# Kernel optimization log

Measured on AMD Instinct MI355X. Metric: run time of the kernel, lower is better.

## Reference

```python
import jax, jax.numpy as jnp
import numpy as np

EPS = 1e-08
PARTIAL_NORM = 1.5
TOPK = 8
SELF_MOD_STEPS = 2


def _layernorm(x, g, b, eps=1e-05):
    mu = jnp.mean(x, axis=-1, keepdims=True)
    var = jnp.mean((x - mu) ** 2, axis=-1, keepdims=True)
    return (x - mu) / jnp.sqrt(var + eps) * g + b


def _spectral_normalize(w, iters=10):
    # mimic torch spectral_norm: divide by top singular value (power iteration)
    u = jnp.ones((w.shape[0],), w.dtype) / np.sqrt(w.shape[0])
    def step(u, _):
        v = w.T @ u
        v = v / (jnp.linalg.norm(v) + 1e-12)
        u2 = w @ v
        u2 = u2 / (jnp.linalg.norm(u2) + 1e-12)
        return u2, None
    u, _ = jax.lax.scan(step, u, None, length=iters)
    v = w.T @ u
    v = v / (jnp.linalg.norm(v) + 1e-12)
    sigma = u @ (w @ v)
    return w / sigma


def setup_inputs() -> dict:
    B, D, H, S, C = 8192, 2048, 1024, 3, 1000
    P = 1024  # proj_dim = ((max(H, D//2)+7)//8)*8
    key = jax.random.key(0)
    ks = jax.random.split(key, 16)
    x = jax.random.normal(ks[0], (B, D), jnp.float32)
    proj_w = jax.random.normal(ks[1], (P, D), jnp.float32) / np.sqrt(D)
    proj_b = jnp.zeros((P,), jnp.float32)
    ln_p_g = jnp.ones((P,), jnp.float32)
    ln_p_b = jnp.zeros((P,), jnp.float32)
    wf_w = jax.random.normal(ks[2], (S, 2 * H, P), jnp.float32) / np.sqrt(P)
    wf_w = jax.vmap(_spectral_normalize)(wf_w)
    wf_b = jax.random.normal(ks[3], (S, 2 * H), jnp.float32) * 0.02
    ln_g = jnp.ones((S, 2 * H), jnp.float32)
    ln_b = jnp.zeros((S, 2 * H), jnp.float32)
    temperature = jnp.ones((1,), jnp.float32)
    phases = jax.random.normal(ks[4], (S, 1), jnp.float32) * 0.5
    gate_w = jax.random.normal(ks[5], (H, H), jnp.float32) / np.sqrt(H)
    gate_b = jnp.zeros((H,), jnp.float32)
    cls_w1 = jax.random.normal(ks[6], (H, H), jnp.float32) / np.sqrt(H)
    cls_b1 = jnp.zeros((H,), jnp.float32)
    cls_w2 = jax.random.normal(ks[7], (C, H), jnp.float32) / np.sqrt(H)
    cls_b2 = jnp.zeros((C,), jnp.float32).at[1].set(0.75)
    return {"x": x, "proj_w": proj_w, "proj_b": proj_b, "ln_p_g": ln_p_g,
            "ln_p_b": ln_p_b, "wf_w": wf_w, "wf_b": wf_b, "ln_g": ln_g,
            "ln_b": ln_b, "temperature": temperature, "phases": phases,
            "gate_w": gate_w, "gate_b": gate_b, "cls_w1": cls_w1,
            "cls_b1": cls_b1, "cls_w2": cls_w2, "cls_b2": cls_b2}


def reference(x, proj_w, proj_b, ln_p_g, ln_p_b, wf_w, wf_b, ln_g, ln_b,
              temperature, phases, gate_w, gate_b, cls_w1, cls_b1, cls_w2, cls_b2):
    H = wf_w.shape[1] // 2
    # input projection (dropout is identity at eval)
    h = jax.nn.gelu(_layernorm(x @ proj_w.T + proj_b, ln_p_g, ln_p_b), approximate=False)
    # all wavefunctions at once: [B, S, 2H]
    out = jnp.einsum('bp,sep->bse', h, wf_w) + wf_b[None]
    out = _layernorm(out, ln_g[None], ln_b[None])
    out = jnp.exp(-out * out)  # ArcBell
    alpha, beta = out[..., :H], out[..., H:]
    norm_sq = jnp.sum(alpha ** 2 + beta ** 2, axis=-1, keepdims=True) + EPS
    factor = jnp.sqrt(PARTIAL_NORM ** 2 / norm_sq)
    alpha = alpha * factor
    beta = beta * factor
    phase = phases[None]  # [1, S, 1]
    c, s = jnp.cos(phase), jnp.sin(phase)
    wave_r = alpha * c - beta * s  # [B, S, H]
    wave_i = alpha * s + beta * c
    # cosine-similarity interference weights
    mean_real = jnp.mean(wave_r, axis=1)  # [B, H]
    mean_norm = jnp.sqrt(jnp.sum(mean_real ** 2, axis=-1, keepdims=True)) + EPS  # [B,1]
    wave_norms = jnp.sqrt(jnp.sum(wave_r ** 2, axis=-1, keepdims=True)) + EPS  # [B,S,1]
    dot = jnp.sum(wave_r * mean_real[:, None], axis=-1, keepdims=True)  # [B,S,1]
    cos_sim = (dot / (wave_norms * mean_norm[:, None]))[..., 0]  # [B,S]
    w = jax.nn.softmax(cos_sim / temperature, axis=1)[..., None]  # [B,S,1]
    sup_r = jnp.sum(wave_r * w, axis=1)  # [B,H]
    sup_i = jnp.sum(wave_i * w, axis=1)
    # self-modulation with leaky residual
    for _ in range(SELF_MOD_STEPS):
        mag = jnp.sqrt(sup_r ** 2 + sup_i ** 2 + EPS)
        gate = jax.nn.sigmoid(mag @ gate_w.T + gate_b)
        sup_r = sup_r * gate + sup_r * 0.1
        sup_i = sup_i * gate + sup_i * 0.1
    mag_sq = sup_r ** 2 + sup_i ** 2
    # top-k mask + scatter + renormalize
    _, inds = jax.lax.top_k(mag_sq, TOPK)
    rows = jnp.arange(mag_sq.shape[0])[:, None]
    mask = jnp.zeros_like(mag_sq).at[rows, inds].set(1.0)
    masked = mag_sq * mask
    probs = masked / (jnp.sum(masked, axis=-1, keepdims=True) + EPS)
    # classifier (dropout identity at eval)
    hid = jax.nn.gelu(probs @ cls_w1.T + cls_b1, approximate=False)
    logits = hid @ cls_w2.T + cls_b2
    return logits
```

## Files before the change

kernel.cpp:

```cpp
#include <hip/hip_runtime.h>
#include <cstdint>

typedef __attribute__((ext_vector_type(8))) __bf16 bf16x8;
typedef __attribute__((ext_vector_type(4))) __bf16 bf16x4;
typedef __attribute__((ext_vector_type(4))) float f32x4;
typedef unsigned long long u64;

__device__ __forceinline__ void gld_lds16(const void* g, void* l) {
  __builtin_amdgcn_global_load_lds(
      (const __attribute__((address_space(1))) void*)g,
      (__attribute__((address_space(3))) void*)l, 16, 0, 0);
}

__device__ __forceinline__ float block_sum(float v, float* scr) {
#pragma unroll
  for (int off = 32; off > 0; off >>= 1) v += __shfl_down(v, off, 64);
  const int w = threadIdx.x >> 6;
  __syncthreads();
  if ((threadIdx.x & 63) == 0) scr[w] = v;
  __syncthreads();
  float s = 0.f;
  const int nw = blockDim.x >> 6;
  for (int i = 0; i < nw; ++i) s += scr[i];
  return s;
}

__device__ __forceinline__ float gelu_fast(float x) {
  const float ax = fabsf(x) * 0.70710678118654752f;
  const float t = 1.f / (1.f + 0.3275911f * ax);
  const float e = __expf(-ax * ax);
  float poly = 1.061405429f;
  poly = poly * t - 1.453152027f;
  poly = poly * t + 1.421413741f;
  poly = poly * t - 0.284496736f;
  poly = poly * t + 0.254829592f;
  const float erfax = 1.f - poly * t * e;
  const float er = copysignf(erfax, x);
  return 0.5f * x * (1.f + er);
}

__global__ __launch_bounds__(256) void k_cast_bf16(const float* __restrict__ in,
                                                   __bf16* __restrict__ out) {
  const long i = ((long)blockIdx.x * 256 + threadIdx.x) * 4;
  f32x4 v = *(const f32x4*)(in + i);
  bf16x4 o = {(__bf16)v[0], (__bf16)v[1], (__bf16)v[2], (__bf16)v[3]};
  *(bf16x4*)(out + i) = o;
}

__global__ __launch_bounds__(256) void k_cast_pad(const float* __restrict__ in,
                                                  __bf16* __restrict__ out,
                                                  int rows_real, int cols) {
  const long i = ((long)blockIdx.x * 256 + threadIdx.x) * 4;
  const int row = (int)(i / cols);
  const int col = (int)(i % cols);
  bf16x4 o;
  if (row < rows_real) {
    f32x4 v = *(const f32x4*)(in + (long)row * cols + col);
    o = (bf16x4){(__bf16)v[0], (__bf16)v[1], (__bf16)v[2], (__bf16)v[3]};
  } else {
    o = (bf16x4){(__bf16)0.f, (__bf16)0.f, (__bf16)0.f, (__bf16)0.f};
  }
  *(bf16x4*)(out + i) = o;
}

__global__ __launch_bounds__(256) void k_transpose1k(const float* __restrict__ in,
                                                     float* __restrict__ out) {
  __shared__ float t[32][33];
  const int tx = threadIdx.x & 31;
  const int ty = threadIdx.x >> 5;
  const int r0 = blockIdx.y * 32, c0 = blockIdx.x * 32;
#pragma unroll
  for (int k = 0; k < 4; ++k)
    t[ty + 8 * k][tx] = in[(long)(r0 + ty + 8 * k) * 1024 + c0 + tx];
  __syncthreads();
#pragma unroll
  for (int k = 0; k < 4; ++k)
    out[(long)(c0 + ty + 8 * k) * 1024 + r0 + tx] = t[tx][ty + 8 * k];
}

__global__ __launch_bounds__(512, 1) void k_gemm256_bt(
    const __bf16* __restrict__ A, const __bf16* __restrict__ B,
    const float* __restrict__ bias, __bf16* __restrict__ C,
    int M, int N, int K) {
  __shared__ __align__(16) __bf16 lds[2][2][256 * 64];
  const int tid = threadIdx.x;
  const int lane = tid & 63;
  const int wid = tid >> 6;
  const int wr = wid >> 2;
  const int wc = wid & 3;
  const int gx = gridDim.x, gy = gridDim.y;
  const int nwg = gx * gy;
  const int lin = blockIdx.y * gx + blockIdx.x;
  const int cpx = nwg >> 3;
  const int wsw = (lin & 7) * cpx + (lin >> 3);
  const int bx = wsw / gy, by = wsw % gy;
  const int m0 = by * 256, n0 = bx * 256;
  const int fr = lane & 15;
  const int fx = lane >> 4;
  const int px = lane & 7;

  const __bf16* Abase = A + (long)m0 * K;
  const __bf16* Bbase = B + (long)n0 * K;

  auto stage_q = [&](int slot, int kt, int mat, int half) {
    const __bf16* src = (mat ? Bbase : Abase) + kt * 64;
#pragma unroll
    for (int q = 0; q < 2; ++q) {
      const int idx = q * 512 + tid;
      const int r = idx >> 3;
      const int pblk = idx & 7;
      const int row = half * 128 + r;
      const int lblk = pblk ^ (r & 7);
      gld_lds16(src + (long)row * K + lblk * 8,
                (char*)&lds[slot][mat][row * 64 + pblk * 8]);
    }
  };
  auto frag = [&](int slot, int mat, int row, int ks) -> bf16x8 {
    return *(const bf16x8*)&lds[slot][mat][row * 64 + ((((ks << 2) + fx) ^ px) << 3)];
  };

  f32x4 acc[8][4] = {};
  const int nt = K >> 6;
#pragma unroll
  for (int qp = 0; qp < 4; ++qp) stage_q(0, 0, qp >> 1, qp & 1);

  const int arow = wr * 128 + fr;
  const int brow = wc * 64 + fr;

  for (int t = 0; t < nt; ++t) {
    const int sc = t & 1, sn = sc ^ 1;
    if (t + 1 < nt) {
#pragma unroll
      for (int qp = 0; qp < 4; ++qp) stage_q(sn, t + 1, qp >> 1, qp & 1);
      asm volatile("s_waitcnt vmcnt(8)" ::: "memory");
    } else {
      asm volatile("s_waitcnt vmcnt(0)" ::: "memory");
    }
    __builtin_amdgcn_sched_barrier(0);
    __builtin_amdgcn_s_barrier();
    bf16x8 b0[4], b1[4];
#pragma unroll
    for (int j = 0; j < 4; ++j) {
      b0[j] = frag(sc, 1, brow + j * 16, 0);
      b1[j] = frag(sc, 1, brow + j * 16, 1);
    }
    __builtin_amdgcn_s_setprio(1);
#pragma unroll
    for (int im = 0; im < 8; ++im) {
      bf16x8 x0 = frag(sc, 0, arow + im * 16, 0);
      bf16x8 x1 = frag(sc, 0, arow + im * 16, 1);
#pragma unroll
      for (int j = 0; j < 4; ++j) {
        acc[im][j] = __builtin_amdgcn_mfma_f32_16x16x32_bf16(x0, b0[j], acc[im][j], 0, 0, 0);
        acc[im][j] = __builtin_amdgcn_mfma_f32_16x16x32_bf16(x1, b1[j], acc[im][j], 0, 0, 0);
      }
    }
    __builtin_amdgcn_s_setprio(0);
    __builtin_amdgcn_s_barrier();
  }

  const int crow0 = m0 + wr * 128 + fx * 4;
  const int ccol0 = n0 + wc * 64 + fr;
#pragma unroll
  for (int j = 0; j < 4; ++j) {
    const int col = ccol0 + j * 16;
    const float bv = bias[col];
#pragma unroll
    for (int im = 0; im < 8; ++im)
#pragma unroll
      for (int r = 0; r < 4; ++r)
        C[(long)(crow0 + im * 16 + r) * N + col] = (__bf16)(acc[im][j][r] + bv);
  }
}

template <int EPI, int BM>
__global__ __launch_bounds__(256) void k_gemm_bt(
    const __bf16* __restrict__ A, const __bf16* __restrict__ B,
    const float* __restrict__ bias, void* __restrict__ Cout,
    int M, int N, int K, int Nreal,
    float* __restrict__ supR, float* __restrict__ supI,
    __bf16* __restrict__ magOut) {
  constexpr int MR = BM / 32;
  __shared__ __align__(16) __bf16 As[2][BM * 32];
  __shared__ __align__(16) __bf16 Bs[2][128 * 32];
  const int tid = threadIdx.x;
  const int lane = tid & 63;
  const int wid = tid >> 6;
  const int wr = wid >> 1, wc = wid & 1;

  const int gx = gridDim.x, gy = gridDim.y;
  const int nwg = gx * gy;
  int bx, by;
  if ((nwg & 7) == 0) {
    const int lin = blockIdx.y * gx + blockIdx.x;
    const int cpx = nwg >> 3;
    const int w = (lin & 7) * cpx + (lin >> 3);
    bx = w / gy;
    by = w % gy;
  } else {
    bx = blockIdx.x;
    by = blockIdx.y;
  }
  const int m0 = by * BM;
  const int n0 = bx * 128;
  const int frow = lane & 15;
  const int fk = (lane >> 4) * 8;
  f32x4 acc[MR][4] = {};

  auto stage = [&](int buf, int k0) {
    const __bf16* Ab = A + (long)m0 * K + k0;
    const __bf16* Bb = B + (long)n0 * K + k0;
#pragma unroll
    for (int q = 0; q < BM / 64; ++q) {
      const int idx = q * 256 + tid;
      const int row = idx >> 2;
      const int col = (idx & 3) * 8;
      gld_lds16(Ab + (long)row * K + col, (char*)(&As[buf][0]) + idx * 16);
    }
#pragma unroll
    for (int q = 0; q < 2; ++q) {
      const int idx = q * 256 + tid;
      const int row = idx >> 2;
      const int col = (idx & 3) * 8;
      gld_lds16(Bb + (long)row * K + col, (char*)(&Bs[buf][0]) + idx * 16);
    }
  };

  const int nt = K >> 5;
  int cur = 0;
  stage(0, 0);
  __syncthreads();
  for (int t = 0; t < nt; ++t) {
    if (t + 1 < nt) stage(cur ^ 1, (t + 1) << 5);
    bf16x8 af[MR], bfr[4];
#pragma unroll
    for (int i = 0; i < MR; ++i)
      af[i] = *(const bf16x8*)(&As[cur][0] + (wr * (BM / 2) + i * 16 + frow) * 32 + fk);
#pragma unroll
    for (int i = 0; i < 4; ++i)
      bfr[i] = *(const bf16x8*)(&Bs[cur][0] + (wc * 64 + i * 16 + frow) * 32 + fk);
#pragma unroll
    for (int im = 0; im < MR; ++im)
#pragma unroll
      for (int in = 0; in < 4; ++in)
        acc[im][in] = __builtin_amdgcn_mfma_f32_16x16x32_bf16(af[im], bfr[in],
                                                              acc[im][in], 0, 0, 0);
    __syncthreads();
    cur ^= 1;
  }

  const int crow0 = m0 + wr * (BM / 2) + (lane >> 4) * 4;
  const int ccol0 = n0 + wc * 64 + (lane & 15);
#pragma unroll
  for (int in = 0; in < 4; ++in) {
    const int col = ccol0 + in * 16;
    if (col >= Nreal) continue;
    const float bv = bias[col];
#pragma unroll
    for (int im = 0; im < MR; ++im) {
#pragma unroll
      for (int r = 0; r < 4; ++r) {
        const long row = crow0 + im * 16 + r;
        const float v = acc[im][in][r] + bv;
        if (EPI == 0) {
          ((float*)Cout)[row * Nreal + col] = v;
        } else if (EPI == 1) {
          ((__bf16*)Cout)[row * Nreal + col] = (__bf16)v;
        } else {
          const float gmul = 1.f / (1.f + __expf(-v)) + 0.1f;
          const long ix = row * Nreal + col;
          const float nr = supR[ix] * gmul;
          const float ni = supI[ix] * gmul;
          supR[ix] = nr;
          supI[ix] = ni;
          if (EPI == 5) magOut[ix] = (__bf16)sqrtf(nr * nr + ni * ni + 1e-8f);
        }
      }
    }
  }
}

__global__ __launch_bounds__(256) void k_ln_gelu(const float* __restrict__ y,
                                                 const float* __restrict__ g,
                                                 const float* __restrict__ b,
                                                 __bf16* __restrict__ h) {
  __shared__ float scr[8];
  const int tid = threadIdx.x;
  const long row = blockIdx.x;
  const float* yr = y + row * 1024;
  f32x4 v = *(const f32x4*)(yr + tid * 4);
  float ls = v[0] + v[1] + v[2] + v[3];
  const float mu = block_sum(ls, scr) * (1.f / 1024.f);
  float lss = 0.f;
#pragma unroll
  for (int j = 0; j < 4; ++j) {
    const float d = v[j] - mu;
    lss += d * d;
  }
  const float var = block_sum(lss, scr) * (1.f / 1024.f);
  const float rstd = rsqrtf(var + 1e-5f);
  bf16x4 o;
#pragma unroll
  for (int j = 0; j < 4; ++j) {
    const int c = tid * 4 + j;
    const float t = (v[j] - mu) * rstd * g[c] + b[c];
    o[j] = (__bf16)gelu_fast(t);
  }
  *(bf16x4*)(h + row * 1024 + tid * 4) = o;
}

__global__ __launch_bounds__(256) void k_stage_c(
    const __bf16* __restrict__ outb, const float* __restrict__ ln_g,
    const float* __restrict__ ln_b, const float* __restrict__ phases,
    const float* __restrict__ temp, float* __restrict__ supr,
    float* __restrict__ supi, __bf16* __restrict__ magp, int b0) {
  __shared__ float wrs[3][1024];
  __shared__ float wis[3][1024];
  __shared__ float gbuf[2048];
  __shared__ float scr[8];
  const int tid = threadIdx.x;
  const long b = blockIdx.x;

#pragma unroll 1
  for (int s = 0; s < 3; ++s) {
    const __bf16* src = outb + b * 6144 + s * 2048;
    bf16x8 v8 = *(const bf16x8*)(src + tid * 8);
    float x[8];
#pragma unroll
    for (int j = 0; j < 8; ++j) x[j] = (float)v8[j];
    float ls = 0.f;
#pragma unroll
    for (int j = 0; j < 8; ++j) ls += x[j];
    const float mu = block_sum(ls, scr) * (1.f / 2048.f);
    float lss = 0.f;
#pragma unroll
    for (int j = 0; j < 8; ++j) {
      const float d = x[j] - mu;
      lss += d * d;
    }
    const float var = block_sum(lss, scr) * (1.f / 2048.f);
    const float rstd = rsqrtf(var + 1e-5f);
    const float* lg = ln_g + s * 2048;
    const float* lb = ln_b + s * 2048;
    float nsq = 0.f;
#pragma unroll
    for (int j = 0; j < 8; ++j) {
      const int e = tid * 8 + j;
      const float yv = (x[j] - mu) * rstd * lg[e] + lb[e];
      const float gv = __expf(-yv * yv);
      gbuf[e] = gv;
      nsq += gv * gv;
    }
    const float normsq = block_sum(nsq, scr) + 1e-8f;
    const float factor = sqrtf(2.25f / normsq);
    const float ph = phases[s];
    const float cs = cosf(ph), sn = sinf(ph);
#pragma unroll
    for (int j = 0; j < 4; ++j) {
      const int h = j * 256 + tid;
      const float a = gbuf[h] * factor;
      const float bb = gbuf[h + 1024] * factor;
      wrs[s][h] = a * cs - bb * sn;
      wis[s][h] = a * sn + bb * cs;
    }
    __syncthreads();
  }

  float mr[4];
  float pmn = 0.f;
#pragma unroll
  for (int j = 0; j < 4; ++j) {
    const int h = j * 256 + tid;
    const float m = (wrs[0][h] + wrs[1][h] + wrs[2][h]) * (1.f / 3.f);
    mr[j] = m;
    pmn += m * m;
  }
  const float mnorm = sqrtf(block_sum(pmn, scr)) + 1e-8f;
  float csim[3];
#pragma unroll 1
  for (int s = 0; s < 3; ++s) {
    float pd = 0.f, pw = 0.f;
#pragma unroll
    for (int j = 0; j < 4; ++j) {
      const int h = j * 256 + tid;
      const float w = wrs[s][h];
      pd += w * mr[j];
      pw += w * w;
    }
    const float dot = block_sum(pd, scr);
    const float wn = sqrtf(block_sum(pw, scr)) + 1e-8f;
    csim[s] = dot / (wn * mnorm);
  }
  const float T = temp[0];
  const float t0 = csim[0] / T, t1 = csim[1] / T, t2 = csim[2] / T;
  const float mx = fmaxf(t0, fmaxf(t1, t2));
  const float e0 = __expf(t0 - mx), e1 = __expf(t1 - mx), e2 = __expf(t2 - mx);
  const float inv = 1.f / (e0 + e1 + e2);
  const float w0 = e0 * inv, w1 = e1 * inv, w2 = e2 * inv;
#pragma unroll
  for (int j = 0; j < 4; ++j) {
    const int h = j * 256 + tid;
    const float sr = wrs[0][h] * w0 + wrs[1][h] * w1 + wrs[2][h] * w2;
    const float si = wis[0][h] * w0 + wis[1][h] * w1 + wis[2][h] * w2;
    supr[(long)(b0 + b) * 1024 + h] = sr;
    supi[(long)(b0 + b) * 1024 + h] = si;
    if (magp) magp[(long)(b0 + b) * 1024 + h] = (__bf16)sqrtf(sr * sr + si * si + 1e-8f);
  }
}

__global__ __launch_bounds__(256) void k_mag(const float* __restrict__ sr,
                                             const float* __restrict__ si,
                                             __bf16* __restrict__ mag) {
  const long i = ((long)blockIdx.x * 256 + threadIdx.x) * 4;
  f32x4 r = *(const f32x4*)(sr + i);
  f32x4 im = *(const f32x4*)(si + i);
  bf16x4 o;
#pragma unroll
  for (int j = 0; j < 4; ++j)
    o[j] = (__bf16)sqrtf(r[j] * r[j] + im[j] * im[j] + 1e-8f);
  *(bf16x4*)(mag + i) = o;
}

__global__ __launch_bounds__(256) void k_topk_cls1(
    const float* __restrict__ supr, const float* __restrict__ supi,
    const float* __restrict__ w1t, const float* __restrict__ b1,
    __bf16* __restrict__ hid) {
  __shared__ u64 candk[32];
  __shared__ u64 selk_s[8];
  __shared__ float ssum_s;
  const int tid = threadIdx.x;
  const int lane = tid & 63;
  const int wv = tid >> 6;
  const long b = blockIdx.x;

  f32x4 r = *(const f32x4*)(supr + b * 1024 + tid * 4);
  f32x4 im = *(const f32x4*)(supi + b * 1024 + tid * 4);
  u64 key[4];
#pragma unroll
  for (int j = 0; j < 4; ++j) {
    const float v = r[j] * r[j] + im[j] * im[j];
    key[j] = ((u64)__float_as_uint(v) << 32) | (unsigned)(~(unsigned)(tid * 4 + j));
  }
  u64 lm = key[0];
  int jm = 0;
#pragma unroll
  for (int j = 1; j < 4; ++j)
    if (key[j] > lm) { lm = key[j]; jm = j; }

#pragma unroll 1
  for (int it = 0; it < 8; ++it) {
    u64 bk = lm;
#pragma unroll
    for (int m = 1; m < 64; m <<= 1) {
      const u64 ok = __shfl_xor(bk, m, 64);
      bk = ok > bk ? ok : bk;
    }
    if (lane == 0) candk[wv * 8 + it] = bk;
    if (bk == lm) {
      key[jm] = 0ULL;
      lm = key[0]; jm = 0;
#pragma unroll
      for (int j = 1; j < 4; ++j)
        if (key[j] > lm) { lm = key[j]; jm = j; }
    }
  }
  __syncthreads();

  if (wv == 0) {
    u64 ck = (lane < 32) ? candk[lane] : 0ULL;
    float ss = 0.f;
#pragma unroll 1
    for (int it = 0; it < 8; ++it) {
      u64 bk = ck;
#pragma unroll
      for (int m = 1; m < 64; m <<= 1) {
        const u64 ok = __shfl_xor(bk, m, 64);
        bk = ok > bk ? ok : bk;
      }
      if (ck == bk) ck = 0ULL;
      if (lane == 0) {
        selk_s[it] = bk;
        ss += __uint_as_float((unsigned)(bk >> 32));
      }
    }
    if (lane == 0) ssum_s = ss;
  }
  __syncthreads();

  const float denom = 1.f / (ssum_s + 1e-8f);
  float p[8];
  int idx[8];
#pragma unroll
  for (int k = 0; k < 8; ++k) {
    const u64 kk = selk_s[k];
    p[k] = __uint_as_float((unsigned)(kk >> 32)) * denom;
    idx[k] = (int)(~(unsigned)kk & 1023u);
  }

  const int o0 = tid * 4;
  float acc0 = b1[o0], acc1 = b1[o0 + 1], acc2 = b1[o0 + 2], acc3 = b1[o0 + 3];
#pragma unroll
  for (int k = 0; k < 8; ++k) {
    const f32x4 wrow = *(const f32x4*)(w1t + (long)idx[k] * 1024 + o0);
    acc0 += p[k] * wrow[0];
    acc1 += p[k] * wrow[1];
    acc2 += p[k] * wrow[2];
    acc3 += p[k] * wrow[3];
  }
  bf16x4 o = {(__bf16)gelu_fast(acc0), (__bf16)gelu_fast(acc1),
              (__bf16)gelu_fast(acc2), (__bf16)gelu_fast(acc3)};
  *(bf16x4*)(hid + b * 1024 + o0) = o;
}

extern "C" void kernel_launch(void* const* d_in, const int* in_sizes, int n_in,
                              void* d_out, int out_size, void* d_ws, size_t ws_size,
                              hipStream_t stream) {
  const float* x      = (const float*)d_in[0];
  const float* proj_w = (const float*)d_in[1];
  const float* proj_b = (const float*)d_in[2];
  const float* ln_p_g = (const float*)d_in[3];
  const float* ln_p_b = (const float*)d_in[4];
  const float* wf_w   = (const float*)d_in[5];
  const float* wf_b   = (const float*)d_in[6];
  const float* ln_g   = (const float*)d_in[7];
  const float* ln_b   = (const float*)d_in[8];
  const float* temperature = (const float*)d_in[9];
  const float* phases = (const float*)d_in[10];
  const float* gate_w = (const float*)d_in[11];
  const float* gate_b = (const float*)d_in[12];
  const float* cls_w1 = (const float*)d_in[13];
  const float* cls_b1 = (const float*)d_in[14];
  const float* cls_w2 = (const float*)d_in[15];
  const float* cls_b2 = (const float*)d_in[16];
  float* out = (float*)d_out;
  (void)in_sizes; (void)n_in; (void)out_size;

  char* ws = (char*)d_ws;
  const size_t MB = 1024 * 1024;

  if (ws_size >= 196 * MB) {
    __bf16* xb    = (__bf16*)(ws + 0);
    float*  supr  = (float*)(ws + 0);
    float*  y1    = (float*)(ws + 32 * MB);
    float*  supi  = (float*)(ws + 32 * MB);
    __bf16* outb  = (__bf16*)(ws + 64 * MB);
    __bf16* magb2 = (__bf16*)(ws + 64 * MB);
    __bf16* hid   = (__bf16*)(ws + 80 * MB);
    float*  w1t   = (float*)(ws + 96 * MB);
    __bf16* hb    = (__bf16*)(ws + 160 * MB);
    __bf16* magb  = (__bf16*)(ws + 160 * MB);
    __bf16* wfwb  = (__bf16*)(ws + 176 * MB);
    __bf16* gwb   = (__bf16*)(ws + 188 * MB);
    __bf16* c2b   = (__bf16*)(ws + 190 * MB);
    __bf16* w1b   = (__bf16*)(ws + 192 * MB);

    k_cast_bf16<<<16384, 256, 0, stream>>>(x, xb);
    k_cast_bf16<<<2048, 256, 0, stream>>>(proj_w, w1b);
    k_cast_bf16<<<6144, 256, 0, stream>>>(wf_w, wfwb);
    k_cast_bf16<<<1024, 256, 0, stream>>>(gate_w, gwb);
    k_cast_pad<<<1024, 256, 0, stream>>>(cls_w2, c2b, 1000, 1024);

    k_gemm_bt<0, 64><<<dim3(8, 128), 256, 0, stream>>>(xb, w1b, proj_b, y1, 8192, 1024, 2048, 1024, nullptr, nullptr, nullptr);
    k_ln_gelu<<<8192, 256, 0, stream>>>(y1, ln_p_g, ln_p_b, hb);

    k_gemm256_bt<<<dim3(24, 32), 512, 0, stream>>>(hb, wfwb, wf_b, outb, 8192, 6144, 1024);
    k_stage_c<<<8192, 256, 0, stream>>>(outb, ln_g, ln_b, phases, temperature, supr, supi, magb, 0);

    k_transpose1k<<<dim3(32, 32), 256, 0, stream>>>(cls_w1, w1t);
    k_gemm_bt<5, 64><<<dim3(8, 128), 256, 0, stream>>>(magb, gwb, gate_b, nullptr, 8192, 1024, 1024, 1024, supr, supi, magb2);
    k_gemm_bt<4, 64><<<dim3(8, 128), 256, 0, stream>>>(magb2, gwb, gate_b, nullptr, 8192, 1024, 1024, 1024, supr, supi, nullptr);

    k_topk_cls1<<<8192, 256, 0, stream>>>(supr, supi, w1t, cls_b1, hid);
    k_gemm_bt<0, 64><<<dim3(8, 128), 256, 0, stream>>>(hid, c2b, cls_b2, out, 8192, 1024, 1024, 1000, nullptr, nullptr, nullptr);
  } else {
    __bf16* xb    = (__bf16*)(ws + 0);
    float*  supr  = (float*)(ws + 0);
    float*  y1    = (float*)(ws + 32 * MB);
    __bf16* outc  = (__bf16*)(ws + 32 * MB);
    __bf16* magb  = (__bf16*)(ws + 32 * MB);
    __bf16* hid   = (__bf16*)(ws + 32 * MB);
    __bf16* w1b   = (__bf16*)(ws + 64 * MB);
    float*  supi  = (float*)(ws + 64 * MB);
    __bf16* wfwb  = (__bf16*)(ws + 96 * MB);
    __bf16* hb    = (__bf16*)(ws + 108 * MB);
    float*  w1t   = (float*)(ws + 108 * MB);
    __bf16* gwb   = (__bf16*)(ws + 124 * MB);
    __bf16* c2b   = (__bf16*)(ws + 126 * MB);

    k_cast_bf16<<<16384, 256, 0, stream>>>(x, xb);
    k_cast_bf16<<<2048, 256, 0, stream>>>(proj_w, w1b);
    k_cast_bf16<<<6144, 256, 0, stream>>>(wf_w, wfwb);
    k_cast_bf16<<<1024, 256, 0, stream>>>(gate_w, gwb);
    k_cast_pad<<<1024, 256, 0, stream>>>(cls_w2, c2b, 1000, 1024);

    k_gemm_bt<0, 64><<<dim3(8, 128), 256, 0, stream>>>(xb, w1b, proj_b, y1, 8192, 1024, 2048, 1024, nullptr, nullptr, nullptr);
    k_ln_gelu<<<8192, 256, 0, stream>>>(y1, ln_p_g, ln_p_b, hb);

    for (int c = 0; c < 4; ++c) {
      k_gemm_bt<1, 128><<<dim3(48, 16), 256, 0, stream>>>(hb + (size_t)c * 2048 * 1024, wfwb, wf_b,
                                                          outc, 2048, 6144, 1024, 6144, nullptr, nullptr, nullptr);
      k_stage_c<<<2048, 256, 0, stream>>>(outc, ln_g, ln_b, phases, temperature,
                                          supr, supi, nullptr, c * 2048);
    }

    k_transpose1k<<<dim3(32, 32), 256, 0, stream>>>(cls_w1, w1t);
    for (int it = 0; it < 2; ++it) {
      k_mag<<<8192, 256, 0, stream>>>(supr, supi, magb);
      k_gemm_bt<4, 64><<<dim3(8, 128), 256, 0, stream>>>(magb, gwb, gate_b, nullptr, 8192, 1024, 1024, 1024, supr, supi, nullptr);
    }
    k_topk_cls1<<<8192, 256, 0, stream>>>(supr, supi, w1t, cls_b1, hid);
    k_gemm_bt<0, 64><<<dim3(8, 128), 256, 0, stream>>>(hid, c2b, cls_b2, out, 8192, 1024, 1024, 1000, nullptr, nullptr, nullptr);
  }
}
```

Baseline: 540.0 us.

## Track squared magnitude instead of real/imag parts through gating; merge weight casts

Because both real and imaginary parts are scaled by the same gate, only their squared magnitude is needed downstream. The code therefore stores a single msq array and scales it by the squared gate factor. This halves the epilogue read/write traffic in the gating GEMMs, removes the separate k_mag kernel in the fallback path, and shrinks the top-k input read. The three weight-cast launches are also merged into one kernel. Computing mag as sqrt(m2+eps) instead of sqrt(r^2+i^2+eps) gives the same math, with slightly different rounding.

```diff
diff --git a/kernel.cpp b/kernel.cpp
--- a/kernel.cpp
+++ b/kernel.cpp
@@ -42,6 +42,23 @@
 __global__ __launch_bounds__(256) void k_cast_bf16(const float* __restrict__ in,
                                                    __bf16* __restrict__ out) {
   const long i = ((long)blockIdx.x * 256 + threadIdx.x) * 4;
+  f32x4 v = *(const f32x4*)(in + i);
+  bf16x4 o = {(__bf16)v[0], (__bf16)v[1], (__bf16)v[2], (__bf16)v[3]};
+  *(bf16x4*)(out + i) = o;
+}
+
+__global__ __launch_bounds__(256) void k_cast_weights(
+    const float* __restrict__ pw, __bf16* __restrict__ w1b,
+    const float* __restrict__ wfw, __bf16* __restrict__ wfwb,
+    const float* __restrict__ gw, __bf16* __restrict__ gwb) {
+  const int bid = blockIdx.x;
+  const float* in;
+  __bf16* out;
+  long base;
+  if (bid < 2048) { in = pw; out = w1b; base = (long)bid * 1024; }
+  else if (bid < 8192) { in = wfw; out = wfwb; base = (long)(bid - 2048) * 1024; }
+  else { in = gw; out = gwb; base = (long)(bid - 8192) * 1024; }
+  const long i = base + threadIdx.x * 4;
   f32x4 v = *(const f32x4*)(in + i);
   bf16x4 o = {(__bf16)v[0], (__bf16)v[1], (__bf16)v[2], (__bf16)v[3]};
   *(bf16x4*)(out + i) = o;
@@ -178,8 +195,7 @@
     const __bf16* __restrict__ A, const __bf16* __restrict__ B,
     const float* __restrict__ bias, void* __restrict__ Cout,
     int M, int N, int K, int Nreal,
-    float* __restrict__ supR, float* __restrict__ supI,
-    __bf16* __restrict__ magOut) {
+    float* __restrict__ msq, __bf16* __restrict__ magOut) {
   constexpr int MR = BM / 32;
   __shared__ __align__(16) __bf16 As[2][BM * 32];
   __shared__ __align__(16) __bf16 Bs[2][128 * 32];
@@ -267,13 +283,11 @@
         } else if (EPI == 1) {
           ((__bf16*)Cout)[row * Nreal + col] = (__bf16)v;
         } else {
-          const float gmul = 1.f / (1.f + __expf(-v)) + 0.1f;
+          const float f = 1.f / (1.f + __expf(-v)) + 0.1f;
           const long ix = row * Nreal + col;
-          const float nr = supR[ix] * gmul;
-          const float ni = supI[ix] * gmul;
-          supR[ix] = nr;
-          supI[ix] = ni;
-          if (EPI == 5) magOut[ix] = (__bf16)sqrtf(nr * nr + ni * ni + 1e-8f);
+          const float m2 = msq[ix] * (f * f);
+          msq[ix] = m2;
+          if (EPI == 6) magOut[ix] = (__bf16)sqrtf(m2 + 1e-8f);
         }
       }
     }
@@ -312,8 +326,8 @@
 __global__ __launch_bounds__(256) void k_stage_c(
     const __bf16* __restrict__ outb, const float* __restrict__ ln_g,
     const float* __restrict__ ln_b, const float* __restrict__ phases,
-    const float* __restrict__ temp, float* __restrict__ supr,
-    float* __restrict__ supi, __bf16* __restrict__ magp, int b0) {
+    const float* __restrict__ temp, float* __restrict__ msq,
+    __bf16* __restrict__ mag0, int b0) {
   __shared__ float wrs[3][1024];
   __shared__ float wis[3][1024];
   __shared__ float gbuf[2048];
@@ -402,27 +416,14 @@
     const int h = j * 256 + tid;
     const float sr = wrs[0][h] * w0 + wrs[1][h] * w1 + wrs[2][h] * w2;
     const float si = wis[0][h] * w0 + wis[1][h] * w1 + wis[2][h] * w2;
-    supr[(long)(b0 + b) * 1024 + h] = sr;
-    supi[(long)(b0 + b) * 1024 + h] = si;
-    if (magp) magp[(long)(b0 + b) * 1024 + h] = (__bf16)sqrtf(sr * sr + si * si + 1e-8f);
-  }
-}
-
-__global__ __launch_bounds__(256) void k_mag(const float* __restrict__ sr,
-                                             const float* __restrict__ si,
-                                             __bf16* __restrict__ mag) {
-  const long i = ((long)blockIdx.x * 256 + threadIdx.x) * 4;
-  f32x4 r = *(const f32x4*)(sr + i);
-  f32x4 im = *(const f32x4*)(si + i);
-  bf16x4 o;
-#pragma unroll
-  for (int j = 0; j < 4; ++j)
-    o[j] = (__bf16)sqrtf(r[j] * r[j] + im[j] * im[j] + 1e-8f);
-  *(bf16x4*)(mag + i) = o;
+    const float m2 = sr * sr + si * si;
+    msq[(long)(b0 + b) * 1024 + h] = m2;
+    mag0[(long)(b0 + b) * 1024 + h] = (__bf16)sqrtf(m2 + 1e-8f);
+  }
 }
 
 __global__ __launch_bounds__(256) void k_topk_cls1(
-    const float* __restrict__ supr, const float* __restrict__ supi,
+    const float* __restrict__ msq,
     const float* __restrict__ w1t, const float* __restrict__ b1,
     __bf16* __restrict__ hid) {
   __shared__ u64 candk[32];
@@ -433,14 +434,11 @@
   const int wv = tid >> 6;
   const long b = blockIdx.x;
 
-  f32x4 r = *(const f32x4*)(supr + b * 1024 + tid * 4);
-  f32x4 im = *(const f32x4*)(supi + b * 1024 + tid * 4);
+  f32x4 mv = *(const f32x4*)(msq + b * 1024 + tid * 4);
   u64 key[4];
 #pragma unroll
-  for (int j = 0; j < 4; ++j) {
-    const float v = r[j] * r[j] + im[j] * im[j];
-    key[j] = ((u64)__float_as_uint(v) << 32) | (unsigned)(~(unsigned)(tid * 4 + j));
-  }
+  for (int j = 0; j < 4; ++j)
+    key[j] = ((u64)__float_as_uint(mv[j]) << 32) | (unsigned)(~(unsigned)(tid * 4 + j));
   u64 lm = key[0];
   int jm = 0;
 #pragma unroll
@@ -539,76 +537,70 @@
   const size_t MB = 1024 * 1024;
 
   if (ws_size >= 196 * MB) {
-    __bf16* xb    = (__bf16*)(ws + 0);
-    float*  supr  = (float*)(ws + 0);
-    float*  y1    = (float*)(ws + 32 * MB);
-    float*  supi  = (float*)(ws + 32 * MB);
-    __bf16* outb  = (__bf16*)(ws + 64 * MB);
-    __bf16* magb2 = (__bf16*)(ws + 64 * MB);
-    __bf16* hid   = (__bf16*)(ws + 80 * MB);
-    float*  w1t   = (float*)(ws + 96 * MB);
-    __bf16* hb    = (__bf16*)(ws + 160 * MB);
-    __bf16* magb  = (__bf16*)(ws + 160 * MB);
-    __bf16* wfwb  = (__bf16*)(ws + 176 * MB);
-    __bf16* gwb   = (__bf16*)(ws + 188 * MB);
-    __bf16* c2b   = (__bf16*)(ws + 190 * MB);
-    __bf16* w1b   = (__bf16*)(ws + 192 * MB);
+    __bf16* xb   = (__bf16*)(ws + 0);
+    float*  msq  = (float*)(ws + 0);
+    float*  y1   = (float*)(ws + 32 * MB);
+    __bf16* mag0 = (__bf16*)(ws + 32 * MB);
+    __bf16* mag1 = (__bf16*)(ws + 48 * MB);
+    __bf16* outb = (__bf16*)(ws + 64 * MB);
+    __bf16* hid  = (__bf16*)(ws + 64 * MB);
+    float*  w1t  = (float*)(ws + 96 * MB);
+    __bf16* hb   = (__bf16*)(ws + 160 * MB);
+    __bf16* wfwb = (__bf16*)(ws + 176 * MB);
+    __bf16* gwb  = (__bf16*)(ws + 188 * MB);
+    __bf16* c2b  = (__bf16*)(ws + 190 * MB);
+    __bf16* w1b  = (__bf16*)(ws + 192 * MB);
 
     k_cast_bf16<<<16384, 256, 0, stream>>>(x, xb);
-    k_cast_bf16<<<2048, 256, 0, stream>>>(proj_w, w1b);
-    k_cast_bf16<<<6144, 256, 0, stream>>>(wf_w, wfwb);
-    k_cast_bf16<<<1024, 256, 0, stream>>>(gate_w, gwb);
+    k_cast_weights<<<9216, 256, 0, stream>>>(proj_w, w1b, wf_w, wfwb, gate_w, gwb);
     k_cast_pad<<<1024, 256, 0, stream>>>(cls_w2, c2b, 1000, 1024);
 
-    k_gemm_bt<0, 64><<<dim3(8, 128), 256, 0, stream>>>(xb, w1b, proj_b, y1, 8192, 1024, 2048, 1024, nullptr, nullptr, nullptr);
+    k_gemm_bt<0, 64><<<dim3(8, 128), 256, 0, stream>>>(xb, w1b, proj_b, y1, 8192, 1024, 2048, 1024, nullptr, nullptr);
     k_ln_gelu<<<8192, 256, 0, stream>>>(y1, ln_p_g, ln_p_b, hb);
 
     k_gemm256_bt<<<dim3(24, 32), 512, 0, stream>>>(hb, wfwb, wf_b, outb, 8192, 6144, 1024);
-    k_stage_c<<<8192, 256, 0, stream>>>(outb, ln_g, ln_b, phases, temperature, supr, supi, magb, 0);
+    k_stage_c<<<8192, 256, 0, stream>>>(outb, ln_g, ln_b, phases, temperature, msq, mag0, 0);
 
     k_transpose1k<<<dim3(32, 32), 256, 0, stream>>>(cls_w1, w1t);
-    k_gemm_bt<5, 64><<<dim3(8, 128), 256, 0, stream>>>(magb, gwb, gate_b, nullptr, 8192, 1024, 1024, 1024, supr, supi, magb2);
-    k_gemm_bt<4, 64><<<dim3(8, 128), 256, 0, stream>>>(magb2, gwb, gate_b, nullptr, 8192, 1024, 1024, 1024, supr, supi, nullptr);
-
-    k_topk_cls1<<<8192, 256, 0, stream>>>(supr, supi, w1t, cls_b1, hid);
-    k_gemm_bt<0, 64><<<dim3(8, 128), 256, 0, stream>>>(hid, c2b, cls_b2, out, 8192, 1024, 1024, 1000, nullptr, nullptr, nullptr);
+    k_gemm_bt<6, 64><<<dim3(8, 128), 256, 0, stream>>>(mag0, gwb, gate_b, nullptr, 8192, 1024, 1024, 1024, msq, mag1);
+    k_gemm_bt<7, 64><<<dim3(8, 128), 256, 0, stream>>>(mag1, gwb, gate_b, nullptr, 8192, 1024, 1024, 1024, msq, nullptr);
+
+    k_topk_cls1<<<8192, 256, 0, stream>>>(msq, w1t, cls_b1, hid);
+    k_gemm_bt<0, 64><<<dim3(8, 128), 256, 0, stream>>>(hid, c2b, cls_b2, out, 8192, 1024, 1024, 1000, nullptr, nullptr);
   } else {
-    __bf16* xb    = (__bf16*)(ws + 0);
-    float*  supr  = (float*)(ws + 0);
-    float*  y1    = (float*)(ws + 32 * MB);
-    __bf16* outc  = (__bf16*)(ws + 32 * MB);
-    __bf16* magb  = (__bf16*)(ws + 32 * MB);
-    __bf16* hid   = (__bf16*)(ws + 32 * MB);
-    __bf16* w1b   = (__bf16*)(ws + 64 * MB);
-    float*  supi  = (float*)(ws + 64 * MB);
-    __bf16* wfwb  = (__bf16*)(ws + 96 * MB);
-    __bf16* hb    = (__bf16*)(ws + 108 * MB);
-    float*  w1t   = (float*)(ws + 108 * MB);
-    __bf16* gwb   = (__bf16*)(ws + 124 * MB);
-    __bf16* c2b   = (__bf16*)(ws + 126 * MB);
+    __bf16* xb   = (__bf16*)(ws + 0);
+    float*  msq  = (float*)(ws + 0);
+    float*  y1   = (float*)(ws + 32 * MB);
+    __bf16* outc = (__bf16*)(ws + 32 * MB);
+    __bf16* mag1 = (__bf16*)(ws + 32 * MB);
+    __bf16* hid  = (__bf16*)(ws + 48 * MB);
+    __bf16* w1b  = (__bf16*)(ws + 64 * MB);
+    __bf16* mag0 = (__bf16*)(ws + 64 * MB);
+    __bf16* wfwb = (__bf16*)(ws + 96 * MB);
+    __bf16* hb   = (__bf16*)(ws + 108 * MB);
+    float*  w1t  = (float*)(ws + 108 * MB);
+    __bf16* gwb  = (__bf16*)(ws + 124 * MB);
+    __bf16* c2b  = (__bf16*)(ws + 126 * MB);
 
     k_cast_bf16<<<16384, 256, 0, stream>>>(x, xb);
-    k_cast_bf16<<<2048, 256, 0, stream>>>(proj_w, w1b);
-    k_cast_bf16<<<6144, 256, 0, stream>>>(wf_w, wfwb);
-    k_cast_bf16<<<1024, 256, 0, stream>>>(gate_w, gwb);
+    k_cast_weights<<<9216, 256, 0, stream>>>(proj_w, w1b, wf_w, wfwb, gate_w, gwb);
     k_cast_pad<<<1024, 256, 0, stream>>>(cls_w2, c2b, 1000, 1024);
 
-    k_gemm_bt<0, 64><<<dim3(8, 128), 256, 0, stream>>>(xb, w1b, proj_b, y1, 8192, 1024, 2048, 1024, nullptr, nullptr, nullptr);
+    k_gemm_bt<0, 64><<<dim3(8, 128), 256, 0, stream>>>(xb, w1b, proj_b, y1, 8192, 1024, 2048, 1024, nullptr, nullptr);
     k_ln_gelu<<<8192, 256, 0, stream>>>(y1, ln_p_g, ln_p_b, hb);
 
     for (int c = 0; c < 4; ++c) {
       k_gemm_bt<1, 128><<<dim3(48, 16), 256, 0, stream>>>(hb + (size_t)c * 2048 * 1024, wfwb, wf_b,
-                                                          outc, 2048, 6144, 1024, 6144, nullptr, nullptr, nullptr);
+                                                          outc, 2048, 6144, 1024, 6144, nullptr, nullptr);
       k_stage_c<<<2048, 256, 0, stream>>>(outc, ln_g, ln_b, phases, temperature,
-                                          supr, supi, nullptr, c * 2048);
+                                          msq, mag0, c * 2048);
     }
 
     k_transpose1k<<<dim3(32, 32), 256, 0, stream>>>(cls_w1, w1t);
-    for (int it = 0; it < 2; ++it) {
-      k_mag<<<8192, 256, 0, stream>>>(supr, supi, magb);
-      k_gemm_bt<4, 64><<<dim3(8, 128), 256, 0, stream>>>(magb, gwb, gate_b, nullptr, 8192, 1024, 1024, 1024, supr, supi, nullptr);
-    }
-    k_topk_cls1<<<8192, 256, 0, stream>>>(supr, supi, w1t, cls_b1, hid);
-    k_gemm_bt<0, 64><<<dim3(8, 128), 256, 0, stream>>>(hid, c2b, cls_b2, out, 8192, 1024, 1024, 1000, nullptr, nullptr, nullptr);
-  }
-}
+    k_gemm_bt<6, 64><<<dim3(8, 128), 256, 0, stream>>>(mag0, gwb, gate_b, nullptr, 8192, 1024, 1024, 1024, msq, mag1);
+    k_gemm_bt<7, 64><<<dim3(8, 128), 256, 0, stream>>>(mag1, gwb, gate_b, nullptr, 8192, 1024, 1024, 1024, msq, nullptr);
+
+    k_topk_cls1<<<8192, 256, 0, stream>>>(msq, w1t, cls_b1, hid);
+    k_gemm_bt<0, 64><<<dim3(8, 128), 256, 0, stream>>>(hid, c2b, cls_b2, out, 8192, 1024, 1024, 1000, nullptr, nullptr);
+  }
+}
```

Measured after the change: 504.7 us. -6.5%, faster.
